# Performance work log

Measured on AMD Instinct MI355X. Metric: run time of the kernel, lower is better.

Reference implementation:

```python
import jax, jax.numpy as jnp
import numpy as np

TEMPERATURE = 30.0


def _adaptive_pool_28(sk):
    # sk: [b, 1, H, W] with H, W divisible by 28 -> [b, 1, 28, 28]
    b, c, h, w = sk.shape
    fh, fw = h // 28, w // 28
    return sk.reshape(b, c, 28, fh, 28, fw).mean(axis=(3, 5))


def setup_inputs() -> dict:
    key = jax.random.key(0)
    ks = jax.random.split(key, 6)
    bs, C, H, W, K = 8, 256, 64, 64, 16
    return {
        "x": jax.random.normal(ks[0], (bs, C, H, W), dtype=jnp.float32),
        "scene_knowledge": jax.random.normal(ks[1], (bs, 1, 56, 56), dtype=jnp.float32),
        "weight": jax.random.normal(ks[2], (K, C, C, 3, 3), dtype=jnp.float32) * 0.02,
        "bias": jax.random.normal(ks[3], (K, C), dtype=jnp.float32) * 0.02,
        "att_w1": jax.random.normal(ks[4], (196, 784), dtype=jnp.float32) * 0.05,
        "att_w2": jax.random.normal(ks[5], (16, 196), dtype=jnp.float32) * 0.05,
    }


def reference(x, scene_knowledge, weight, bias, att_w1, att_w2):
    bs, C, h, w = x.shape
    K = weight.shape[0]

    # ---- Attention: pooled scene knowledge -> softmax over K experts ----
    pooled = _adaptive_pool_28(scene_knowledge).reshape(bs, 28 * 28)  # [bs, 784]
    hdn = jax.nn.relu(pooled @ att_w1.T)                               # [bs, 196]
    logits = hdn @ att_w2.T                                            # [bs, K]
    att = jax.nn.softmax(logits / TEMPERATURE, axis=-1)                # [bs, K]

    # ---- Aggregate per-sample conv weights and biases ----
    agg_w = jnp.einsum("bk,koihw->boihw", att, weight)  # [bs, C, C, 3, 3]
    agg_b = att @ bias                                   # [bs, C]

    # ---- Per-sample conv (equivalent to groups=bs trick in torch) ----
    def per_sample_conv(xi, wi):
        # xi: [C, h, w], wi: [C, C, 3, 3]
        return jax.lax.conv_general_dilated(
            xi[None], wi, window_strides=(1, 1), padding="SAME",
            dimension_numbers=("NCHW", "OIHW", "NCHW"))[0]

    out = jax.vmap(per_sample_conv)(x, agg_w)            # [bs, C, h, w]
    out = out + agg_b[:, :, None, None] + x              # bias + residual
    return out
```

## Files before the change

### kernel.cpp

```cpp
#include <hip/hip_runtime.h>
#include <stdint.h>
#include <stddef.h>

typedef __bf16 bf16;
typedef __bf16 bf16x8 __attribute__((ext_vector_type(8)));
typedef __bf16 bf16x4 __attribute__((ext_vector_type(4)));
typedef float f32x4 __attribute__((ext_vector_type(4)));

static_assert(sizeof(bf16x8) == 16, "bf16x8 must be 16B");

__device__ __forceinline__ void gload_lds16(const void* g, void* l) {
    __builtin_amdgcn_global_load_lds(
        (const __attribute__((address_space(1))) uint32_t*)g,
        (__attribute__((address_space(3))) uint32_t*)l, 16, 0, 0);
}

__global__ void attn_kernel(const float* __restrict__ sk,
                            const float* __restrict__ w1,
                            const float* __restrict__ w2,
                            float* __restrict__ att) {
    const int b = blockIdx.x, t = threadIdx.x;
    __shared__ float pooled[784];
    __shared__ float hdn[196];
    __shared__ float logits[16];
    const float* skb = sk + (size_t)b * 3136;
    for (int e = t; e < 784; e += 256) {
        int oy = e / 28, ox = e % 28;
        const float* p = skb + (oy * 2) * 56 + ox * 2;
        pooled[e] = 0.25f * (p[0] + p[1] + p[56] + p[57]);
    }
    __syncthreads();
    if (t < 196) {
        float s = 0.f;
        const float* wr = w1 + (size_t)t * 784;
        for (int i = 0; i < 784; ++i) s += pooled[i] * wr[i];
        hdn[t] = s > 0.f ? s : 0.f;
    }
    __syncthreads();
    if (t < 16) {
        float s = 0.f;
        const float* wr = w2 + (size_t)t * 196;
        for (int j = 0; j < 196; ++j) s += hdn[j] * wr[j];
        logits[t] = s * (1.0f / 30.0f);
    }
    __syncthreads();
    if (t == 0) {
        float m = logits[0];
        for (int k = 1; k < 16; ++k) m = fmaxf(m, logits[k]);
        float e16[16], sum = 0.f;
        for (int k = 0; k < 16; ++k) { e16[k] = expf(logits[k] - m); sum += e16[k]; }
        float inv = 1.f / sum;
        for (int k = 0; k < 16; ++k) att[b * 16 + k] = e16[k] * inv;
    }
}

__global__ __launch_bounds__(256) void agg_kernel(
    const float* __restrict__ weight,
    const float* __restrict__ bias,
    const float* __restrict__ att,
    bf16* __restrict__ aggw,
    float* __restrict__ aggb) {
    const int bid = blockIdx.x;
    const int co = bid & 255, chunk = bid >> 8;
    const int t = threadIdx.x;

    __shared__ bf16 accW[8 * 576];

    if (chunk == 0 && t < 8) {
        float s = 0.f;
        for (int k = 0; k < 16; ++k) s += att[t * 16 + k] * bias[k * 256 + co];
        aggb[t * 256 + co] = s;
    }

    if (t < 144) {
        const float* wbase = weight + (size_t)co * 2304 + (size_t)chunk * 576 + (size_t)t * 4;
        float4 wv[16];
#pragma unroll
        for (int k = 0; k < 16; ++k)
            wv[k] = *(const float4*)(wbase + (size_t)k * 589824);
        float a[8][4];
#pragma unroll
        for (int b = 0; b < 8; ++b)
#pragma unroll
            for (int j = 0; j < 4; ++j) a[b][j] = 0.f;
#pragma unroll
        for (int k = 0; k < 16; ++k) {
#pragma unroll
            for (int b = 0; b < 8; ++b) {
                const float av = att[b * 16 + k];
                a[b][0] += av * wv[k].x;
                a[b][1] += av * wv[k].y;
                a[b][2] += av * wv[k].z;
                a[b][3] += av * wv[k].w;
            }
        }
#pragma unroll
        for (int b = 0; b < 8; ++b) {
            bf16x4 v;
#pragma unroll
            for (int j = 0; j < 4; ++j) v[j] = (bf16)a[b][j];
            *(bf16x4*)&accW[b * 576 + t * 4] = v;
        }
    }
    __syncthreads();

    const int half = co >> 7, co_l = co & 127;
    for (int s = t; s < 576; s += 256) {
        const int b = s / 72, r = s - b * 72;
        const int pos = r >> 3, cg = r & 7;
        bf16x8 v;
#pragma unroll
        for (int c = 0; c < 8; ++c) v[c] = accW[b * 576 + (cg * 8 + c) * 9 + pos];
        size_t o = (((((size_t)b * 9 + pos) * 4 + chunk) * 2 + half) * 8 + cg) * 128 + co_l;
        *(bf16x8*)(aggw + o * 8) = v;
    }
}

__global__ void transpose_kernel(const float* __restrict__ x, bf16* __restrict__ xt) {
    const int bid = blockIdx.x;
    const int b = bid >> 6, y = bid & 63;
    const int t = threadIdx.x;
    __shared__ bf16 T[256 * 64];
    const float* src = x + (size_t)b * 256 * 4096 + (size_t)y * 64;
    for (int i = 0; i < 16; ++i) {
        int v = t + 256 * i;
        int ci = v >> 4, x4 = (v & 15) * 4;
        float4 f = *(const float4*)(src + (size_t)ci * 4096 + x4);
        bf16* d = &T[ci * 64 + x4];
        d[0] = (bf16)f.x; d[1] = (bf16)f.y; d[2] = (bf16)f.z; d[3] = (bf16)f.w;
    }
    __syncthreads();
    bf16* dstb = xt + (size_t)bid * 16384;
    for (int i = 0; i < 8; ++i) {
        int c2 = t + 256 * i;
        int cg = c2 >> 6, xx = c2 & 63;
        bf16x8 v;
#pragma unroll
        for (int c = 0; c < 8; ++c) v[c] = T[(cg * 8 + c) * 64 + xx];
        *(bf16x8*)(dstb + (size_t)c2 * 8) = v;
    }
}

__global__ __launch_bounds__(256, 2) void conv_kernel(
    const bf16* __restrict__ xt, const bf16* __restrict__ aggw,
    const float* __restrict__ aggb, const float* __restrict__ xin,
    float* __restrict__ out) {
    const int bid = blockIdx.x;
    const int ytile = bid & 31;
    const int half = (bid >> 5) & 1;
    const int b = bid >> 6;
    const int tid = threadIdx.x;
    const int wave = tid >> 6, lane = tid & 63;
    const int wm = wave & 1, wn = wave >> 1;
    const int lane15 = lane & 15, quad = lane >> 4;

    __shared__ __align__(16) bf16 Xs[4][8][66][8];
    __shared__ __align__(16) bf16 Ws[2][8][128][8];

    f32x4 acc[4][4];
#pragma unroll
    for (int mt = 0; mt < 4; ++mt)
#pragma unroll
        for (int nt = 0; nt < 4; ++nt) acc[mt][nt] = f32x4{0.f, 0.f, 0.f, 0.f};

    {
        uint4 z; z.x = z.y = z.z = z.w = 0u;
        uint4* p = (uint4*)&Xs[0][0][0][0];
        for (int i = tid; i < 2112; i += 256) p[i] = z;
    }
    __syncthreads();

    const int yrow = ytile * 2 - 1 + wave;
    const bool rowok = (yrow >= 0) && (yrow < 64);
    const bf16* xsrc = xt + ((size_t)b * 64 + (rowok ? yrow : 0)) * 16384 + (size_t)lane * 8;
    bf16* xdstbase = &Xs[wave][0][1][0];

    const bf16* wsrcbase = aggw + (size_t)b * 589824 + (size_t)half * 8192
                         + (size_t)wave * 2048 + (size_t)lane * 8;
    bf16* wslice0 = ((bf16*)&Ws[0][0][0][0]) + wave * 2048;
    bf16* wslice1 = ((bf16*)&Ws[1][0][0][0]) + wave * 2048;

    if (rowok) {
#pragma unroll
        for (int cg = 0; cg < 8; ++cg)
            gload_lds16(xsrc + cg * 512, xdstbase + cg * 528);
    }
#pragma unroll
    for (int i = 0; i < 4; ++i)
        gload_lds16(wsrcbase + i * 512, wslice0 + i * 512);
    asm volatile("s_waitcnt vmcnt(0)" ::: "memory");
    __builtin_amdgcn_s_barrier();

    for (int chunk = 0; chunk < 4; ++chunk) {
#pragma unroll
        for (int pos = 0; pos < 9; ++pos) {
            const int bufp = (chunk + pos) & 1;
            bf16* wnext = bufp ? wslice0 : wslice1;
            if (pos < 8) {
                const bf16* s0 = wsrcbase + (size_t)(pos + 1) * 65536 + (size_t)chunk * 16384;
#pragma unroll
                for (int i = 0; i < 4; ++i)
                    gload_lds16(s0 + i * 512, wnext + i * 512);
            } else if (chunk < 3) {
                const bf16* s0 = wsrcbase + (size_t)(chunk + 1) * 16384;
#pragma unroll
                for (int i = 0; i < 4; ++i)
                    gload_lds16(s0 + i * 512, wnext + i * 512);
            }
            const int kh = pos / 3, kw = pos - kh * 3;
            const int xr = wn + kh;
            const bf16* wcur = (const bf16*)&Ws[bufp][0][0][0];
#pragma unroll
            for (int s = 0; s < 2; ++s) {
                const int cg = s * 4 + quad;
                bf16x8 afr[4], bfr[4];
#pragma unroll
                for (int mt = 0; mt < 4; ++mt)
                    afr[mt] = *(const bf16x8*)(wcur + (size_t)cg * 1024
                                               + (size_t)(wm * 64 + mt * 16 + lane15) * 8);
#pragma unroll
                for (int nt = 0; nt < 4; ++nt)
                    bfr[nt] = *(const bf16x8*)&Xs[xr][cg][kw + nt * 16 + lane15][0];
#pragma unroll
                for (int mt = 0; mt < 4; ++mt)
#pragma unroll
                    for (int nt = 0; nt < 4; ++nt)
                        acc[mt][nt] = __builtin_amdgcn_mfma_f32_16x16x32_bf16(
                            afr[mt], bfr[nt], acc[mt][nt], 0, 0, 0);
            }
            if (chunk < 3 || pos < 8) {
                asm volatile("s_waitcnt vmcnt(0) lgkmcnt(0)" ::: "memory");
                __builtin_amdgcn_s_barrier();
            }
        }
        if (chunk < 3) {
            if (rowok) {
                const bf16* s0 = xsrc + (size_t)(chunk + 1) * 4096;
#pragma unroll
                for (int cg = 0; cg < 8; ++cg)
                    gload_lds16(s0 + cg * 512, xdstbase + cg * 528);
            }
            asm volatile("s_waitcnt vmcnt(0)" ::: "memory");
            __builtin_amdgcn_s_barrier();
        }
    }

    const int y = ytile * 2 + wn;
#pragma unroll
    for (int mt = 0; mt < 4; ++mt) {
#pragma unroll
        for (int r = 0; r < 4; ++r) {
            const int co = half * 128 + wm * 64 + mt * 16 + quad * 4 + r;
            const float bbv = aggb[b * 256 + co];
            const size_t rowbase = (((size_t)b * 256 + co) * 64 + y) * 64;
#pragma unroll
            for (int nt = 0; nt < 4; ++nt) {
                const size_t oidx = rowbase + nt * 16 + lane15;
                out[oidx] = acc[mt][nt][r] + bbv + xin[oidx];
            }
        }
    }
}

extern "C" void kernel_launch(void* const* d_in, const int* in_sizes, int n_in,
                              void* d_out, int out_size, void* d_ws, size_t ws_size,
                              hipStream_t stream) {
    const float* x    = (const float*)d_in[0];
    const float* sk   = (const float*)d_in[1];
    const float* wgt  = (const float*)d_in[2];
    const float* bias = (const float*)d_in[3];
    const float* w1   = (const float*)d_in[4];
    const float* w2   = (const float*)d_in[5];
    float* out = (float*)d_out;

    char* ws = (char*)d_ws;
    float* att  = (float*)(ws + 0);
    float* aggb = (float*)(ws + 1024);
    bf16*  aggw = (bf16*)(ws + 16384);
    bf16*  xt   = (bf16*)(ws + 16384 + 9437184);

    attn_kernel<<<8, 256, 0, stream>>>(sk, w1, w2, att);
    agg_kernel<<<1024, 256, 0, stream>>>(wgt, bias, att, aggw, aggb);
    transpose_kernel<<<512, 256, 0, stream>>>(x, xt);
    conv_kernel<<<512, 256, 0, stream>>>(xt, aggw, aggb, x, out);
}
```

Before: 199.1 us.

## Load conv weights directly into registers and parallelize attention matvecs

The conv kernel no longer stages per-sample weights through a double-buffered LDS tile. Each lane prefetches its MFMA A-fragments straight from global memory into a double-buffered register array, which removes most per-position barriers and frees LDS. Block indexing is reordered so consecutive blocks share y-tiles across samples and halves. The attention kernel moves to 1024 threads, with 16-lane cooperative dot products and shuffle reductions in place of serial per-thread loops. The trade-offs are more registers and uncoalesced 16-byte global loads per lane, which may hurt occupancy or latency hiding.

```diff
diff --git a/kernel.cpp b/kernel.cpp
--- a/kernel.cpp
+++ b/kernel.cpp
@@ -15,33 +15,47 @@
         (__attribute__((address_space(3))) uint32_t*)l, 16, 0, 0);
 }
 
-__global__ void attn_kernel(const float* __restrict__ sk,
-                            const float* __restrict__ w1,
-                            const float* __restrict__ w2,
-                            float* __restrict__ att) {
+__global__ __launch_bounds__(1024) void attn_kernel(const float* __restrict__ sk,
+                                                    const float* __restrict__ w1,
+                                                    const float* __restrict__ w2,
+                                                    float* __restrict__ att) {
     const int b = blockIdx.x, t = threadIdx.x;
     __shared__ float pooled[784];
     __shared__ float hdn[196];
     __shared__ float logits[16];
     const float* skb = sk + (size_t)b * 3136;
-    for (int e = t; e < 784; e += 256) {
-        int oy = e / 28, ox = e % 28;
+    if (t < 784) {
+        int oy = t / 28, ox = t % 28;
         const float* p = skb + (oy * 2) * 56 + ox * 2;
-        pooled[e] = 0.25f * (p[0] + p[1] + p[56] + p[57]);
-    }
-    __syncthreads();
-    if (t < 196) {
+        pooled[t] = 0.25f * (p[0] + p[1] + p[56] + p[57]);
+    }
+    __syncthreads();
+    const int q = t & 15, jg = t >> 4;
+#pragma unroll
+    for (int rep = 0; rep < 4; ++rep) {
+        const int j = rep * 64 + jg;
         float s = 0.f;
-        const float* wr = w1 + (size_t)t * 784;
-        for (int i = 0; i < 784; ++i) s += pooled[i] * wr[i];
-        hdn[t] = s > 0.f ? s : 0.f;
-    }
-    __syncthreads();
-    if (t < 16) {
+        if (j < 196) {
+            const float* wr = w1 + (size_t)j * 784 + q;
+#pragma unroll 7
+            for (int i = 0; i < 49; ++i) s += pooled[q + i * 16] * wr[i * 16];
+        }
+#pragma unroll
+        for (int off = 8; off; off >>= 1) s += __shfl_xor(s, off, 16);
+        if (j < 196 && q == 0) hdn[j] = s > 0.f ? s : 0.f;
+    }
+    __syncthreads();
+    if (t < 256) {
+        const int jj = t >> 4, qq = t & 15;
         float s = 0.f;
-        const float* wr = w2 + (size_t)t * 196;
-        for (int j = 0; j < 196; ++j) s += hdn[j] * wr[j];
-        logits[t] = s * (1.0f / 30.0f);
+#pragma unroll
+        for (int i = 0; i < 13; ++i) {
+            const int idx = qq + i * 16;
+            if (idx < 196) s += hdn[idx] * w2[jj * 196 + idx];
+        }
+#pragma unroll
+        for (int off = 8; off; off >>= 1) s += __shfl_xor(s, off, 16);
+        if (qq == 0) logits[jj] = s * (1.0f / 30.0f);
     }
     __syncthreads();
     if (t == 0) {
@@ -146,16 +160,14 @@
     const float* __restrict__ aggb, const float* __restrict__ xin,
     float* __restrict__ out) {
     const int bid = blockIdx.x;
-    const int ytile = bid & 31;
-    const int half = (bid >> 5) & 1;
-    const int b = bid >> 6;
+    const int slice = bid & 15, ytile = bid >> 4;
+    const int b = slice >> 1, half = slice & 1;
     const int tid = threadIdx.x;
     const int wave = tid >> 6, lane = tid & 63;
     const int wm = wave & 1, wn = wave >> 1;
     const int lane15 = lane & 15, quad = lane >> 4;
 
     __shared__ __align__(16) bf16 Xs[4][8][66][8];
-    __shared__ __align__(16) bf16 Ws[2][8][128][8];
 
     f32x4 acc[4][4];
 #pragma unroll
@@ -175,10 +187,10 @@
     const bf16* xsrc = xt + ((size_t)b * 64 + (rowok ? yrow : 0)) * 16384 + (size_t)lane * 8;
     bf16* xdstbase = &Xs[wave][0][1][0];
 
-    const bf16* wsrcbase = aggw + (size_t)b * 589824 + (size_t)half * 8192
-                         + (size_t)wave * 2048 + (size_t)lane * 8;
-    bf16* wslice0 = ((bf16*)&Ws[0][0][0][0]) + wave * 2048;
-    bf16* wslice1 = ((bf16*)&Ws[1][0][0][0]) + wave * 2048;
+    const bf16* wlane = aggw + (size_t)b * 589824 + (size_t)half * 8192
+                      + (size_t)quad * 1024 + (size_t)(wm * 64 + lane15) * 8;
+
+    bf16x8 afr[2][2][4];
 
     if (rowok) {
 #pragma unroll
@@ -186,38 +198,42 @@
             gload_lds16(xsrc + cg * 512, xdstbase + cg * 528);
     }
 #pragma unroll
-    for (int i = 0; i < 4; ++i)
-        gload_lds16(wsrcbase + i * 512, wslice0 + i * 512);
+    for (int s_ = 0; s_ < 2; ++s_)
+#pragma unroll
+        for (int mt = 0; mt < 4; ++mt)
+            afr[0][s_][mt] = *(const bf16x8*)(wlane + s_ * 4096 + mt * 128);
     asm volatile("s_waitcnt vmcnt(0)" ::: "memory");
     __builtin_amdgcn_s_barrier();
 
-    for (int chunk = 0; chunk < 4; ++chunk) {
-#pragma unroll
-        for (int pos = 0; pos < 9; ++pos) {
-            const int bufp = (chunk + pos) & 1;
-            bf16* wnext = bufp ? wslice0 : wslice1;
-            if (pos < 8) {
-                const bf16* s0 = wsrcbase + (size_t)(pos + 1) * 65536 + (size_t)chunk * 16384;
-#pragma unroll
-                for (int i = 0; i < 4; ++i)
-                    gload_lds16(s0 + i * 512, wnext + i * 512);
-            } else if (chunk < 3) {
-                const bf16* s0 = wsrcbase + (size_t)(chunk + 1) * 16384;
-#pragma unroll
-                for (int i = 0; i < 4; ++i)
-                    gload_lds16(s0 + i * 512, wnext + i * 512);
+    for (int cp = 0; cp < 2; ++cp) {
+#pragma unroll
+        for (int t = 0; t < 18; ++t) {
+            const int par = t & 1;
+            const int pos = t % 9;
+            const int chunk = cp * 2 + t / 9;
+            if (t < 17) {
+                const int npos = (t + 1) % 9;
+                const int nchunk = cp * 2 + (t + 1) / 9;
+                const bf16* pb = wlane + (size_t)npos * 65536 + (size_t)nchunk * 16384;
+#pragma unroll
+                for (int s_ = 0; s_ < 2; ++s_)
+#pragma unroll
+                    for (int mt = 0; mt < 4; ++mt)
+                        afr[par ^ 1][s_][mt] = *(const bf16x8*)(pb + s_ * 4096 + mt * 128);
+            } else if (cp == 0) {
+                const bf16* pb = wlane + (size_t)(cp * 2 + 2) * 16384;
+#pragma unroll
+                for (int s_ = 0; s_ < 2; ++s_)
+#pragma unroll
+                    for (int mt = 0; mt < 4; ++mt)
+                        afr[par ^ 1][s_][mt] = *(const bf16x8*)(pb + s_ * 4096 + mt * 128);
             }
             const int kh = pos / 3, kw = pos - kh * 3;
             const int xr = wn + kh;
-            const bf16* wcur = (const bf16*)&Ws[bufp][0][0][0];
-#pragma unroll
-            for (int s = 0; s < 2; ++s) {
-                const int cg = s * 4 + quad;
-                bf16x8 afr[4], bfr[4];
-#pragma unroll
-                for (int mt = 0; mt < 4; ++mt)
-                    afr[mt] = *(const bf16x8*)(wcur + (size_t)cg * 1024
-                                               + (size_t)(wm * 64 + mt * 16 + lane15) * 8);
+#pragma unroll
+            for (int s_ = 0; s_ < 2; ++s_) {
+                const int cg = s_ * 4 + quad;
+                bf16x8 bfr[4];
 #pragma unroll
                 for (int nt = 0; nt < 4; ++nt)
                     bfr[nt] = *(const bf16x8*)&Xs[xr][cg][kw + nt * 16 + lane15][0];
@@ -226,22 +242,20 @@
 #pragma unroll
                     for (int nt = 0; nt < 4; ++nt)
                         acc[mt][nt] = __builtin_amdgcn_mfma_f32_16x16x32_bf16(
-                            afr[mt], bfr[nt], acc[mt][nt], 0, 0, 0);
-            }
-            if (chunk < 3 || pos < 8) {
-                asm volatile("s_waitcnt vmcnt(0) lgkmcnt(0)" ::: "memory");
+                            afr[par][s_][mt], bfr[nt], acc[mt][nt], 0, 0, 0);
+            }
+            if (pos == 8 && (t == 8 || cp == 0)) {
+                asm volatile("s_waitcnt lgkmcnt(0)" ::: "memory");
                 __builtin_amdgcn_s_barrier();
-            }
-        }
-        if (chunk < 3) {
-            if (rowok) {
-                const bf16* s0 = xsrc + (size_t)(chunk + 1) * 4096;
-#pragma unroll
-                for (int cg = 0; cg < 8; ++cg)
-                    gload_lds16(s0 + cg * 512, xdstbase + cg * 528);
-            }
-            asm volatile("s_waitcnt vmcnt(0)" ::: "memory");
-            __builtin_amdgcn_s_barrier();
+                if (rowok) {
+                    const bf16* s0 = xsrc + (size_t)(chunk + 1) * 4096;
+#pragma unroll
+                    for (int cg = 0; cg < 8; ++cg)
+                        gload_lds16(s0 + cg * 512, xdstbase + cg * 528);
+                }
+                asm volatile("s_waitcnt vmcnt(0)" ::: "memory");
+                __builtin_amdgcn_s_barrier();
+            }
         }
     }
 
@@ -279,7 +293,7 @@
     bf16*  aggw = (bf16*)(ws + 16384);
     bf16*  xt   = (bf16*)(ws + 16384 + 9437184);
 
-    attn_kernel<<<8, 256, 0, stream>>>(sk, w1, w2, att);
+    attn_kernel<<<8, 1024, 0, stream>>>(sk, w1, w2, att);
     agg_kernel<<<1024, 256, 0, stream>>>(wgt, bias, att, aggw, aggb);
     transpose_kernel<<<512, 256, 0, stream>>>(x, xt);
     conv_kernel<<<512, 256, 0, stream>>>(xt, aggw, aggb, x, out);
```

Measured after the change: 198.3 us. Within noise of the previous version (-0.4%).
